# Optimization experiments

Hardware: AMD Instinct MI355X
Metric: run time of the kernel (lower is better)

Reference implementation:

```python
import jax, jax.numpy as jnp
from jax import lax
import numpy as np

LRELU_SLOPE = 0.1
DILATIONS = (1, 2, 4)
B, C, T = 8, 256, 8192


def pd_indexing(x, d, dilation):
    """Pitch-dependent past/future gather along time.
    x: (B, C, T); d: (B, 1, T) float dilation factors.
    Returns xP, xF: (B, C, T), zero where index is out of range.
    """
    b, c, t_len = x.shape
    t = jnp.arange(t_len, dtype=x.dtype)  # (T,)
    dil = d[:, 0, :] * dilation           # (B, T)
    idxP = jnp.round(t[None, :] - dil).astype(jnp.int32)  # (B, T)
    idxF = jnp.round(t[None, :] + dil).astype(jnp.int32)  # (B, T)
    validP = (idxP >= 0).astype(x.dtype)[:, None, :]        # (B,1,T)
    validF = (idxF < t_len).astype(x.dtype)[:, None, :]
    idxPc = jnp.broadcast_to(jnp.clip(idxP, 0, t_len - 1)[:, None, :], (b, c, t_len))
    idxFc = jnp.broadcast_to(jnp.clip(idxF, 0, t_len - 1)[:, None, :], (b, c, t_len))
    xP = jnp.take_along_axis(x, idxPc, axis=2) * validP
    xF = jnp.take_along_axis(x, idxFc, axis=2) * validF
    return xP, xF


def conv1x1(x, w, bias):
    # x: (B,C,T), w: (O,C), bias: (O,)
    return jnp.einsum('oc,bct->bot', w, x) + bias[None, :, None]


def conv3(x, w, bias):
    # x: (B,C,T), w: (O,C,3), padding=1
    y = lax.conv_general_dilated(x, w, window_strides=(1,), padding=[(1, 1)],
                                 dimension_numbers=('NCH', 'OIH', 'NCH'))
    return y + bias[None, :, None]


def setup_inputs() -> dict:
    key = jax.random.key(0)
    ks = jax.random.split(key, 8)
    x = jax.random.normal(ks[0], (B, C, T), dtype=jnp.float32)
    d = jax.random.uniform(ks[1], (B, 1, T), dtype=jnp.float32, minval=0.0, maxval=16.0)
    n = len(DILATIONS)
    s1 = 1.0 / np.sqrt(C)
    s3 = 1.0 / np.sqrt(3 * C)
    WC = jax.random.normal(ks[2], (n, C, C), dtype=jnp.float32) * s1
    WP = jax.random.normal(ks[3], (n, C, C), dtype=jnp.float32) * s1
    WF = jax.random.normal(ks[4], (n, C, C), dtype=jnp.float32) * s1
    WA = jax.random.normal(ks[5], (n, C, C, 3), dtype=jnp.float32) * s3
    bC = jnp.zeros((n, C), dtype=jnp.float32)
    bP = jnp.zeros((n, C), dtype=jnp.float32)
    bF = jnp.zeros((n, C), dtype=jnp.float32)
    bA = jnp.zeros((n, C), dtype=jnp.float32)
    return {"x": x, "d": d, "WC": WC, "bC": bC, "WP": WP, "bP": bP,
            "WF": WF, "bF": bF, "WA": WA, "bA": bA}


def reference(x, d, WC, bC, WP, bP, WF, bF, WA, bA):
    for i, dilation in enumerate(DILATIONS):
        xt = jax.nn.leaky_relu(x, LRELU_SLOPE)
        xP, xF = pd_indexing(xt, d, dilation)
        xt = conv1x1(xt, WC[i], bC[i]) + conv1x1(xP, WP[i], bP[i]) + conv1x1(xF, WF[i], bF[i])
        xt = jax.nn.leaky_relu(xt, LRELU_SLOPE)
        xt = conv3(xt, WA[i], bA[i])
        x = xt + x
    return x
```

## Files before the change

### kernel.cpp

```cpp
#include <hip/hip_runtime.h>
#include <hip/hip_bf16.h>
#include <cstddef>
#include <cstdint>

constexpr int Bn = 8, Cn = 256, Tn = 8192;
constexpr int NL = 3;
constexpr int Kc = 768;
constexpr float SLOPE = 0.1f;

typedef unsigned short u16;
using bf8   = __attribute__((ext_vector_type(8))) short;
using f32x4 = __attribute__((ext_vector_type(4))) float;

__device__ __forceinline__ float lrelu(float v) { return v > 0.f ? v : SLOPE * v; }
__device__ __forceinline__ u16 f2bf(float f) {
    __hip_bfloat16 h = __float2bfloat16(f);
    return *reinterpret_cast<u16*>(&h);
}

__device__ __forceinline__ void g2l16(const u16* g, u16* l) {
    __builtin_amdgcn_global_load_lds(
        (const __attribute__((address_space(1))) char*)g,
        (__attribute__((address_space(3))) char*)l, 16, 0, 0);
}

__device__ __forceinline__ void pipe_barrier() {
    __builtin_amdgcn_s_barrier();
    __builtin_amdgcn_sched_barrier(0);
}

__global__ __launch_bounds__(256)
void k_wprep(const float* __restrict__ WC, const float* __restrict__ WP,
             const float* __restrict__ WF, const float* __restrict__ WA,
             const float* __restrict__ bC, const float* __restrict__ bP,
             const float* __restrict__ bF,
             u16* __restrict__ Wcat, u16* __restrict__ WAp, float* __restrict__ bSum,
             u16* __restrict__ zrow)
{
    if (blockIdx.x == 0) zrow[threadIdx.x] = 0;
    const int n1 = NL * Cn * Kc;
    for (int i = blockIdx.x * blockDim.x + threadIdx.x; i < n1;
         i += gridDim.x * blockDim.x) {
        int c = i % Cn;
        int s = (i / Cn) % 3;
        int o = (i / (3 * Cn)) % Cn;
        int l = i / (3 * Cn * Cn);
        size_t src = ((size_t)l * Cn + o) * Cn + c;
        float wc = (s == 0) ? WC[src] : (s == 1) ? WP[src] : WF[src];
        Wcat[i] = f2bf(wc);
        WAp[i] = f2bf(WA[src * 3 + s]);
    }
    for (int i = blockIdx.x * blockDim.x + threadIdx.x; i < NL * Cn;
         i += gridDim.x * blockDim.x)
        bSum[i] = bC[i] + bP[i] + bF[i];
}

__global__ __launch_bounds__(256)
void k_prep(const float* __restrict__ x, u16* __restrict__ xT)
{
    __shared__ float s[64][65];
    const int b = blockIdx.z, c0 = blockIdx.y * 64, t0 = blockIdx.x * 64;
    const int tid = threadIdx.x;
    const float* xb = x + ((size_t)b * Cn + c0) * Tn + t0;

    int tt = tid & 63, c4 = tid >> 6;
    for (int cc = c4; cc < 64; cc += 4)
        s[cc][tt] = xb[(size_t)cc * Tn + tt];
    __syncthreads();

    int ccS = tid & 63, t4 = tid >> 6;
    u16* xTb = xT + ((size_t)b * Tn + t0) * Cn + c0;
    for (int t2 = t4; t2 < 64; t2 += 4)
        xTb[(size_t)t2 * Cn + ccS] = f2bf(lrelu(s[ccS][t2]));
}

constexpr int SLOT = 12800;
constexpr int ZOFF = 3 * SLOT;
constexpr int ZSZ  = 130 * 256;

__global__ __launch_bounds__(512, 2)
void k_fused(const u16* __restrict__ xTsrc, const float* __restrict__ d,
             const u16* __restrict__ Wl, const float* __restrict__ bS,
             const u16* __restrict__ WAl, const float* __restrict__ bA,
             float dil, const float* __restrict__ xres, float* __restrict__ out,
             u16* __restrict__ xTn, int writeXT, const u16* __restrict__ zrow)
{
    __shared__ u16 smem[ZOFF + ZSZ];
    __shared__ int sRow[3][130];

    const int tid = threadIdx.x;
    const int b = blockIdx.z;
    const int t0 = blockIdx.x * 128;

    if (tid < 130) {
        int tz = t0 - 1 + tid;
        if (tz < 0 || tz >= Tn) {
            sRow[0][tid] = -1; sRow[1][tid] = -1; sRow[2][tid] = -1;
        } else {
            float dv = d[(size_t)b * Tn + tz] * dil;
            int ip = (int)rintf((float)tz - dv);
            int iF = (int)rintf((float)tz + dv);
            sRow[0][tid] = tz;
            sRow[1][tid] = (ip >= 0) ? ip : -1;
            sRow[2][tid] = (iF < Tn) ? iF : -1;
        }
    }
    __syncthreads();

    const int lane = tid & 63, wv = tid >> 6;
    const int srow = tid >> 2;
    const int sg  = ((tid & 3) ^ ((tid >> 3) & 3)) * 8;
    const int sg2 = ((lane & 3) ^ ((lane >> 3) & 3)) * 8;

    const u16* xTb = xTsrc + (size_t)b * Tn * Cn;
    const char* xbc = (const char*)xTb;
    const int zoffA = (int)((const char*)(zrow + sg) - xbc);
    const int zoffB = (int)((const char*)(zrow + sg2) - xbc);

    int offX[3];
    #pragma unroll
    for (int s = 0; s < 3; ++s) {
        int r = sRow[s][srow];
        offX[s] = (r >= 0) ? (int)((r * Cn + sg) * 2) : zoffA;
    }
    int offX2[3] = { zoffB, zoffB, zoffB };
    if (wv == 7) {
        int j = lane >> 2;
        if (j < 2) {
            #pragma unroll
            for (int s = 0; s < 3; ++s) {
                int r = sRow[s][128 + j];
                offX2[s] = (r >= 0) ? (int)((r * Cn + sg2) * 2) : zoffB;
            }
        }
    }
    const u16* wbase1 = Wl  + (size_t)srow * Kc + sg;
    const u16* wbase2 = WAl + (size_t)srow * Kc + sg;

    const int mo  = (wv & 3) * 64;
    const int wzr = (wv >> 2) * 64;
    const bool heavy = (wzr == 64);
    const int lr = lane & 15, quad = lane >> 4;
    const int rchunk = (quad ^ ((lr >> 1) & 3)) * 8;

    auto dma1 = [&](int kg, int slot) {
        int seg = kg >> 3, kk = (kg & 7) * 32;
        u16* bw = smem + slot * SLOT;
        u16* bx = bw + 8192;
        if (wv == 7)
            g2l16((const u16*)(xbc + offX2[seg] + kk * 2), bx + 4096 + lane * 8);
        g2l16(wbase1 + seg * 256 + kk,                    bw + tid * 8);
        g2l16(wbase1 + (size_t)128 * Kc + seg * 256 + kk, bw + 4096 + tid * 8);
        g2l16((const u16*)(xbc + offX[seg] + kk * 2),     bx + tid * 8);
    };
    auto dma2 = [&](int kg, int slot) {
        u16* bw = smem + slot * SLOT;
        g2l16(wbase2 + kg * 32,                    bw + tid * 8);
        g2l16(wbase2 + (size_t)128 * Kc + kg * 32, bw + 4096 + tid * 8);
    };

    const f32x4 zv4 = {0.f, 0.f, 0.f, 0.f};
    f32x4 acc[4][5];
    #pragma unroll
    for (int mi = 0; mi < 4; ++mi)
        #pragma unroll
        for (int ni = 0; ni < 5; ++ni) acc[mi][ni] = zv4;

    dma1(0, 0); dma1(1, 1);

    #pragma unroll
    for (int kg = 0; kg < 24; ++kg) {
        if (kg < 23) {
            if (wv == 7) asm volatile("s_waitcnt vmcnt(4) lgkmcnt(0)" ::: "memory");
            else         asm volatile("s_waitcnt vmcnt(3) lgkmcnt(0)" ::: "memory");
        } else {
            asm volatile("s_waitcnt vmcnt(2) lgkmcnt(0)" ::: "memory");
        }
        pipe_barrier();

        const u16* bW = smem + (kg % 3) * SLOT;
        const u16* bX = bW + 8192;
        bf8 af[4], bg[4], bg4 = {};
        #pragma unroll
        for (int mi = 0; mi < 4; ++mi)
            af[mi] = *(const bf8*)(bW + (mo + mi * 16 + lr) * 32 + rchunk);
        #pragma unroll
        for (int ni = 0; ni < 4; ++ni)
            bg[ni] = *(const bf8*)(bX + (wzr + ni * 16 + lr) * 32 + rchunk);
        if (heavy)
            bg4 = *(const bf8*)(bX + (128 + lr) * 32 + rchunk);

        if (kg + 2 < 24) dma1(kg + 2, (kg + 2) % 3);
        else             dma2(kg - 22, (kg - 22) % 3);

        __builtin_amdgcn_s_setprio(1);
        #pragma unroll
        for (int mi = 0; mi < 4; ++mi)
            #pragma unroll
            for (int ni = 0; ni < 4; ++ni)
                acc[mi][ni] = __builtin_amdgcn_mfma_f32_16x16x32_bf16(
                    af[mi], bg[ni], acc[mi][ni], 0, 0, 0);
        if (heavy) {
            #pragma unroll
            for (int mi = 0; mi < 4; ++mi)
                acc[mi][4] = __builtin_amdgcn_mfma_f32_16x16x32_bf16(
                    af[mi], bg4, acc[mi][4], 0, 0, 0);
        }
        __builtin_amdgcn_s_setprio(0);
    }

    u16* zsm = smem + ZOFF;
    {
        float4 bSv[4];
        #pragma unroll
        for (int mi = 0; mi < 4; ++mi)
            bSv[mi] = *(const float4*)(bS + mo + mi * 16 + quad * 4);

        #pragma unroll
        for (int ni = 0; ni < 4; ++ni) {
            int zr = wzr + ni * 16 + lr;
            int tz = t0 - 1 + zr;
            bool vz = (tz >= 0) && (tz < Tn);
            #pragma unroll
            for (int mi = 0; mi < 4; ++mi) {
                int ob = mo + mi * 16 + quad * 4;
                ushort4 pk;
                #pragma unroll
                for (int r = 0; r < 4; ++r) {
                    float v = acc[mi][ni][r] + ((const float*)&bSv[mi])[r];
                    ((u16*)&pk)[r] = vz ? f2bf(lrelu(v)) : (u16)0;
                }
                int zi = zr * 256 + ((((ob >> 3) ^ (zr & 7)) << 3) | (ob & 7));
                *(ushort4*)(zsm + zi) = pk;
            }
        }
        if (heavy && lr < 2) {
            int zr = 128 + lr;
            int tz = t0 - 1 + zr;
            bool vz = (tz >= 0) && (tz < Tn);
            #pragma unroll
            for (int mi = 0; mi < 4; ++mi) {
                int ob = mo + mi * 16 + quad * 4;
                ushort4 pk;
                #pragma unroll
                for (int r = 0; r < 4; ++r) {
                    float v = acc[mi][4][r] + ((const float*)&bSv[mi])[r];
                    ((u16*)&pk)[r] = vz ? f2bf(lrelu(v)) : (u16)0;
                }
                int zi = zr * 256 + ((((ob >> 3) ^ (zr & 7)) << 3) | (ob & 7));
                *(ushort4*)(zsm + zi) = pk;
            }
        }
    }
    asm volatile("s_waitcnt lgkmcnt(0)" ::: "memory");
    __builtin_amdgcn_s_barrier();
    __builtin_amdgcn_sched_barrier(0);

    #pragma unroll
    for (int mi = 0; mi < 4; ++mi)
        #pragma unroll
        for (int ni = 0; ni < 4; ++ni) acc[mi][ni] = zv4;

    #pragma unroll
    for (int kg = 0; kg < 24; ++kg) {
        if (kg < 23) asm volatile("s_waitcnt vmcnt(2) lgkmcnt(0)" ::: "memory");
        else         asm volatile("s_waitcnt vmcnt(0) lgkmcnt(0)" ::: "memory");
        pipe_barrier();

        const u16* bW = smem + (kg % 3) * SLOT;
        const int tap = kg >> 3, cI = (kg & 7) * 4 + quad;
        bf8 af[4], bg[4];
        #pragma unroll
        for (int mi = 0; mi < 4; ++mi)
            af[mi] = *(const bf8*)(bW + (mo + mi * 16 + lr) * 32 + rchunk);
        #pragma unroll
        for (int ni = 0; ni < 4; ++ni) {
            int zr = wzr + ni * 16 + lr + tap;
            bg[ni] = *(const bf8*)(zsm + zr * 256 + ((cI ^ (zr & 7)) << 3));
        }
        if (kg + 2 < 24) dma2(kg + 2, (kg + 2) % 3);

        __builtin_amdgcn_s_setprio(1);
        #pragma unroll
        for (int mi = 0; mi < 4; ++mi)
            #pragma unroll
            for (int ni = 0; ni < 4; ++ni)
                acc[mi][ni] = __builtin_amdgcn_mfma_f32_16x16x32_bf16(
                    af[mi], bg[ni], acc[mi][ni], 0, 0, 0);
        __builtin_amdgcn_s_setprio(0);
    }

    {
        float4 bAv[4];
        #pragma unroll
        for (int mi = 0; mi < 4; ++mi)
            bAv[mi] = *(const float4*)(bA + mo + mi * 16 + quad * 4);

        #pragma unroll
        for (int mi = 0; mi < 4; ++mi) {
            int ob = mo + mi * 16 + quad * 4;
            #pragma unroll
            for (int ni = 0; ni < 4; ++ni) {
                int t = t0 + wzr + ni * 16 + lr;
                ushort4 px;
                #pragma unroll
                for (int r = 0; r < 4; ++r) {
                    size_t idx = ((size_t)b * Cn + ob + r) * Tn + t;
                    float v = acc[mi][ni][r] + ((const float*)&bAv[mi])[r] + xres[idx];
                    out[idx] = v;
                    ((u16*)&px)[r] = f2bf(lrelu(v));
                }
                if (writeXT)
                    *(ushort4*)(xTn + ((size_t)b * Tn + t) * Cn + ob) = px;
            }
        }
    }
}

extern "C" void kernel_launch(void* const* d_in, const int* in_sizes, int n_in,
                              void* d_out, int out_size, void* d_ws, size_t ws_size,
                              hipStream_t stream)
{
    const float* x  = (const float*)d_in[0];
    const float* d  = (const float*)d_in[1];
    const float* WC = (const float*)d_in[2];
    const float* bC = (const float*)d_in[3];
    const float* WP = (const float*)d_in[4];
    const float* bP = (const float*)d_in[5];
    const float* WF = (const float*)d_in[6];
    const float* bF = (const float*)d_in[7];
    const float* WA = (const float*)d_in[8];
    const float* bA = (const float*)d_in[9];
    float* out = (float*)d_out;

    char* ws = (char*)d_ws;
    u16*   xTa  = (u16*)(ws);
    u16*   xTb  = (u16*)(ws + (size_t)Bn * Tn * Cn * 2);
    u16*   Wcat = (u16*)(ws + (size_t)2 * Bn * Tn * Cn * 2);
    u16*   WAp  = Wcat + (size_t)NL * Cn * Kc;
    float* bSum = (float*)(WAp + (size_t)NL * Cn * Kc);
    u16*   zrow = (u16*)(bSum + NL * Cn);

    k_wprep<<<dim3(1024), dim3(256), 0, stream>>>(WC, WP, WF, WA, bC, bP, bF,
                                                  Wcat, WAp, bSum, zrow);

    dim3 gP(Tn / 64, Cn / 64, Bn);
    k_prep<<<gP, dim3(256), 0, stream>>>(x, xTa);

    const float dils[NL] = {1.f, 2.f, 4.f};
    const float* xcur = x;
    u16* xsrc = xTa;
    u16* xdst = xTb;
    for (int i = 0; i < NL; ++i) {
        k_fused<<<dim3(Tn / 128, 1, Bn), dim3(512), 0, stream>>>(
            xsrc, d,
            Wcat + (size_t)i * Cn * Kc, bSum + (size_t)i * Cn,
            WAp  + (size_t)i * Cn * Kc, bA + (size_t)i * Cn,
            dils[i], xcur, out, xdst, (i < NL - 1) ? 1 : 0, zrow);
        xcur = out;
        u16* tmp = xsrc; xsrc = xdst; xdst = tmp;
    }
}
```

Before: 389.0 us.

## Replace LDS triple-buffered DMA staging with direct register double-buffered global loads

Removes the global_load_lds triple-buffered shared-memory staging of weights and gathered activations in both GEMM phases. Each wave now loads its A (weight) and B (gathered xT rows) fragments straight from global memory into registers, ping-ponging between two register sets. This drops the per-step barriers and the LDS footprint, which could raise occupancy. In exchange it loses cross-wave data sharing: each weight fragment is now fetched by two waves and each activation fragment by four, and register pressure goes up.

```diff
diff --git a/kernel.cpp b/kernel.cpp
--- a/kernel.cpp
+++ b/kernel.cpp
@@ -16,17 +16,6 @@
 __device__ __forceinline__ u16 f2bf(float f) {
     __hip_bfloat16 h = __float2bfloat16(f);
     return *reinterpret_cast<u16*>(&h);
-}
-
-__device__ __forceinline__ void g2l16(const u16* g, u16* l) {
-    __builtin_amdgcn_global_load_lds(
-        (const __attribute__((address_space(1))) char*)g,
-        (__attribute__((address_space(3))) char*)l, 16, 0, 0);
-}
-
-__device__ __forceinline__ void pipe_barrier() {
-    __builtin_amdgcn_s_barrier();
-    __builtin_amdgcn_sched_barrier(0);
 }
 
 __global__ __launch_bounds__(256)
@@ -74,9 +63,7 @@
         xTb[(size_t)t2 * Cn + ccS] = f2bf(lrelu(s[ccS][t2]));
 }
 
-constexpr int SLOT = 12800;
-constexpr int ZOFF = 3 * SLOT;
-constexpr int ZSZ  = 130 * 256;
+constexpr int ZSZ = 130 * 256;
 
 __global__ __launch_bounds__(512, 2)
 void k_fused(const u16* __restrict__ xTsrc, const float* __restrict__ d,
@@ -85,7 +72,7 @@
              float dil, const float* __restrict__ xres, float* __restrict__ out,
              u16* __restrict__ xTn, int writeXT, const u16* __restrict__ zrow)
 {
-    __shared__ u16 smem[ZOFF + ZSZ];
+    __shared__ u16 zsm[ZSZ];
     __shared__ int sRow[3][130];
 
     const int tid = threadIdx.x;
@@ -108,56 +95,36 @@
     __syncthreads();
 
     const int lane = tid & 63, wv = tid >> 6;
-    const int srow = tid >> 2;
-    const int sg  = ((tid & 3) ^ ((tid >> 3) & 3)) * 8;
-    const int sg2 = ((lane & 3) ^ ((lane >> 3) & 3)) * 8;
-
-    const u16* xTb = xTsrc + (size_t)b * Tn * Cn;
-    const char* xbc = (const char*)xTb;
-    const int zoffA = (int)((const char*)(zrow + sg) - xbc);
-    const int zoffB = (int)((const char*)(zrow + sg2) - xbc);
-
-    int offX[3];
-    #pragma unroll
-    for (int s = 0; s < 3; ++s) {
-        int r = sRow[s][srow];
-        offX[s] = (r >= 0) ? (int)((r * Cn + sg) * 2) : zoffA;
-    }
-    int offX2[3] = { zoffB, zoffB, zoffB };
-    if (wv == 7) {
-        int j = lane >> 2;
-        if (j < 2) {
-            #pragma unroll
-            for (int s = 0; s < 3; ++s) {
-                int r = sRow[s][128 + j];
-                offX2[s] = (r >= 0) ? (int)((r * Cn + sg2) * 2) : zoffB;
-            }
-        }
-    }
-    const u16* wbase1 = Wl  + (size_t)srow * Kc + sg;
-    const u16* wbase2 = WAl + (size_t)srow * Kc + sg;
-
     const int mo  = (wv & 3) * 64;
     const int wzr = (wv >> 2) * 64;
     const bool heavy = (wzr == 64);
     const int lr = lane & 15, quad = lane >> 4;
-    const int rchunk = (quad ^ ((lr >> 1) & 3)) * 8;
-
-    auto dma1 = [&](int kg, int slot) {
-        int seg = kg >> 3, kk = (kg & 7) * 32;
-        u16* bw = smem + slot * SLOT;
-        u16* bx = bw + 8192;
-        if (wv == 7)
-            g2l16((const u16*)(xbc + offX2[seg] + kk * 2), bx + 4096 + lane * 8);
-        g2l16(wbase1 + seg * 256 + kk,                    bw + tid * 8);
-        g2l16(wbase1 + (size_t)128 * Kc + seg * 256 + kk, bw + 4096 + tid * 8);
-        g2l16((const u16*)(xbc + offX[seg] + kk * 2),     bx + tid * 8);
-    };
-    auto dma2 = [&](int kg, int slot) {
-        u16* bw = smem + slot * SLOT;
-        g2l16(wbase2 + kg * 32,                    bw + tid * 8);
-        g2l16(wbase2 + (size_t)128 * Kc + kg * 32, bw + 4096 + tid * 8);
-    };
+
+    const u16* xTb = xTsrc + (size_t)b * Tn * Cn;
+    const char* xbc = (const char*)xTb;
+    const int zoffq = (int)((const char*)zrow - xbc) + quad * 16;
+
+    int offB[3][4];
+    #pragma unroll
+    for (int ni = 0; ni < 4; ++ni) {
+        int zr = wzr + ni * 16 + lr;
+        #pragma unroll
+        for (int s = 0; s < 3; ++s) {
+            int r = sRow[s][zr];
+            offB[s][ni] = (r >= 0) ? (r * (Cn * 2) + quad * 16) : zoffq;
+        }
+    }
+    int offH[3] = { zoffq, zoffq, zoffq };
+    if (heavy && lr < 2) {
+        #pragma unroll
+        for (int s = 0; s < 3; ++s) {
+            int r = sRow[s][128 + lr];
+            offH[s] = (r >= 0) ? (r * (Cn * 2) + quad * 16) : zoffq;
+        }
+    }
+
+    const u16* wp1 = Wl  + (size_t)(mo + lr) * Kc + quad * 8;
+    const u16* wp2 = WAl + (size_t)(mo + lr) * Kc + quad * 8;
 
     const f32x4 zv4 = {0.f, 0.f, 0.f, 0.f};
     f32x4 acc[4][5];
@@ -166,50 +133,48 @@
         #pragma unroll
         for (int ni = 0; ni < 5; ++ni) acc[mi][ni] = zv4;
 
-    dma1(0, 0); dma1(1, 1);
-
-    #pragma unroll
-    for (int kg = 0; kg < 24; ++kg) {
-        if (kg < 23) {
-            if (wv == 7) asm volatile("s_waitcnt vmcnt(4) lgkmcnt(0)" ::: "memory");
-            else         asm volatile("s_waitcnt vmcnt(3) lgkmcnt(0)" ::: "memory");
-        } else {
-            asm volatile("s_waitcnt vmcnt(2) lgkmcnt(0)" ::: "memory");
-        }
-        pipe_barrier();
-
-        const u16* bW = smem + (kg % 3) * SLOT;
-        const u16* bX = bW + 8192;
-        bf8 af[4], bg[4], bg4 = {};
-        #pragma unroll
-        for (int mi = 0; mi < 4; ++mi)
-            af[mi] = *(const bf8*)(bW + (mo + mi * 16 + lr) * 32 + rchunk);
-        #pragma unroll
-        for (int ni = 0; ni < 4; ++ni)
-            bg[ni] = *(const bf8*)(bX + (wzr + ni * 16 + lr) * 32 + rchunk);
-        if (heavy)
-            bg4 = *(const bf8*)(bX + (128 + lr) * 32 + rchunk);
-
-        if (kg + 2 < 24) dma1(kg + 2, (kg + 2) % 3);
-        else             dma2(kg - 22, (kg - 22) % 3);
-
-        __builtin_amdgcn_s_setprio(1);
-        #pragma unroll
-        for (int mi = 0; mi < 4; ++mi)
+    {
+        auto loadA = [&](int kg, bf8* a) {
+            #pragma unroll
+            for (int mi = 0; mi < 4; ++mi)
+                a[mi] = *(const bf8*)(wp1 + (size_t)mi * 16 * Kc + kg * 32);
+        };
+        auto loadB = [&](int kg, bf8* bv) {
+            int seg = kg >> 3, kb = (kg & 7) * 64;
             #pragma unroll
             for (int ni = 0; ni < 4; ++ni)
-                acc[mi][ni] = __builtin_amdgcn_mfma_f32_16x16x32_bf16(
-                    af[mi], bg[ni], acc[mi][ni], 0, 0, 0);
-        if (heavy) {
+                bv[ni] = *(const bf8*)(xbc + offB[seg][ni] + kb);
+            if (heavy)
+                bv[4] = *(const bf8*)(xbc + offH[seg] + kb);
+        };
+        auto mm = [&](const bf8* a, const bf8* bv) {
+            __builtin_amdgcn_s_setprio(1);
             #pragma unroll
             for (int mi = 0; mi < 4; ++mi)
-                acc[mi][4] = __builtin_amdgcn_mfma_f32_16x16x32_bf16(
-                    af[mi], bg4, acc[mi][4], 0, 0, 0);
-        }
-        __builtin_amdgcn_s_setprio(0);
-    }
-
-    u16* zsm = smem + ZOFF;
+                #pragma unroll
+                for (int ni = 0; ni < 4; ++ni)
+                    acc[mi][ni] = __builtin_amdgcn_mfma_f32_16x16x32_bf16(
+                        a[mi], bv[ni], acc[mi][ni], 0, 0, 0);
+            if (heavy) {
+                #pragma unroll
+                for (int mi = 0; mi < 4; ++mi)
+                    acc[mi][4] = __builtin_amdgcn_mfma_f32_16x16x32_bf16(
+                        a[mi], bv[4], acc[mi][4], 0, 0, 0);
+            }
+            __builtin_amdgcn_s_setprio(0);
+        };
+
+        bf8 aA[4], bA_[5] = {}, aB[4], bB_[5] = {};
+        loadA(0, aA); loadB(0, bA_);
+        #pragma unroll
+        for (int kg = 0; kg < 24; kg += 2) {
+            loadA(kg + 1, aB); loadB(kg + 1, bB_);
+            mm(aA, bA_);
+            if (kg + 2 < 24) { loadA(kg + 2, aA); loadB(kg + 2, bA_); }
+            mm(aB, bB_);
+        }
+    }
+
     {
         float4 bSv[4];
         #pragma unroll
@@ -252,42 +217,47 @@
             }
         }
     }
-    asm volatile("s_waitcnt lgkmcnt(0)" ::: "memory");
-    __builtin_amdgcn_s_barrier();
-    __builtin_amdgcn_sched_barrier(0);
+    __syncthreads();
 
     #pragma unroll
     for (int mi = 0; mi < 4; ++mi)
         #pragma unroll
         for (int ni = 0; ni < 4; ++ni) acc[mi][ni] = zv4;
 
-    #pragma unroll
-    for (int kg = 0; kg < 24; ++kg) {
-        if (kg < 23) asm volatile("s_waitcnt vmcnt(2) lgkmcnt(0)" ::: "memory");
-        else         asm volatile("s_waitcnt vmcnt(0) lgkmcnt(0)" ::: "memory");
-        pipe_barrier();
-
-        const u16* bW = smem + (kg % 3) * SLOT;
-        const int tap = kg >> 3, cI = (kg & 7) * 4 + quad;
-        bf8 af[4], bg[4];
-        #pragma unroll
-        for (int mi = 0; mi < 4; ++mi)
-            af[mi] = *(const bf8*)(bW + (mo + mi * 16 + lr) * 32 + rchunk);
-        #pragma unroll
-        for (int ni = 0; ni < 4; ++ni) {
-            int zr = wzr + ni * 16 + lr + tap;
-            bg[ni] = *(const bf8*)(zsm + zr * 256 + ((cI ^ (zr & 7)) << 3));
-        }
-        if (kg + 2 < 24) dma2(kg + 2, (kg + 2) % 3);
-
-        __builtin_amdgcn_s_setprio(1);
-        #pragma unroll
-        for (int mi = 0; mi < 4; ++mi)
-            #pragma unroll
-            for (int ni = 0; ni < 4; ++ni)
-                acc[mi][ni] = __builtin_amdgcn_mfma_f32_16x16x32_bf16(
-                    af[mi], bg[ni], acc[mi][ni], 0, 0, 0);
-        __builtin_amdgcn_s_setprio(0);
+    {
+        auto loadA = [&](int kg, bf8* a) {
+            #pragma unroll
+            for (int mi = 0; mi < 4; ++mi)
+                a[mi] = *(const bf8*)(wp2 + (size_t)mi * 16 * Kc + kg * 32);
+        };
+        auto loadB = [&](int kg, bf8* bv) {
+            int tap = kg >> 3, cI = (kg & 7) * 4 + quad;
+            #pragma unroll
+            for (int ni = 0; ni < 4; ++ni) {
+                int zr = wzr + ni * 16 + lr + tap;
+                bv[ni] = *(const bf8*)(zsm + zr * 256 + ((cI ^ (zr & 7)) << 3));
+            }
+        };
+        auto mm = [&](const bf8* a, const bf8* bv) {
+            __builtin_amdgcn_s_setprio(1);
+            #pragma unroll
+            for (int mi = 0; mi < 4; ++mi)
+                #pragma unroll
+                for (int ni = 0; ni < 4; ++ni)
+                    acc[mi][ni] = __builtin_amdgcn_mfma_f32_16x16x32_bf16(
+                        a[mi], bv[ni], acc[mi][ni], 0, 0, 0);
+            __builtin_amdgcn_s_setprio(0);
+        };
+
+        bf8 aA[4], bA_[4], aB[4], bB_[4];
+        loadA(0, aA); loadB(0, bA_);
+        #pragma unroll
+        for (int kg = 0; kg < 24; kg += 2) {
+            loadA(kg + 1, aB); loadB(kg + 1, bB_);
+            mm(aA, bA_);
+            if (kg + 2 < 24) { loadA(kg + 2, aA); loadB(kg + 2, bA_); }
+            mm(aB, bB_);
+        }
     }
 
     {
```

After: 611.4 us. 57.2% more time.
